# Kernel optimization log

Hardware: AMD Instinct MI355X
Metric: run time of the kernel (lower is better)

## Reference

```python
import jax, jax.numpy as jnp
import numpy as np

D = 2048
H = 16
DK = D // H
B = 2
S = 2048


def setup_inputs() -> dict:
    key = jax.random.key(0)
    ks = jax.random.split(key, 11)
    s = 1.0 / np.sqrt(D)
    inp = {
        "q": jax.random.normal(ks[0], (B, S, D), jnp.float32),
        "k": jax.random.normal(ks[1], (B, S, D), jnp.float32),
        "v": jax.random.normal(ks[2], (B, S, D), jnp.float32),
        "mask": 0,
        "Wq": jax.random.normal(ks[3], (D, D), jnp.float32) * s,
        "bq": jax.random.normal(ks[4], (D,), jnp.float32) * s,
        "Wk": jax.random.normal(ks[5], (D, D), jnp.float32) * s,
        "bk": jax.random.normal(ks[6], (D,), jnp.float32) * s,
        "Wv": jax.random.normal(ks[7], (D, D), jnp.float32) * s,
        "bv": jax.random.normal(ks[8], (D,), jnp.float32) * s,
        "Wo": jax.random.normal(ks[9], (D, D), jnp.float32) * s,
        "bo": jax.random.normal(ks[10], (D,), jnp.float32) * s,
    }
    return inp


def reference(q, k, v, mask, Wq, bq, Wk, bk, Wv, bv, Wo, bo):
    # Linear projections (torch Linear: x @ W.T + b)
    query = q @ Wq.T + bq  # [B,S,D]
    key_ = k @ Wk.T + bk
    value = v @ Wv.T + bv
    # split heads -> [B,S,H,DK]
    query = query.reshape(B, S, H, DK)
    key_ = key_.reshape(B, S, H, DK)
    value = value.reshape(B, S, H, DK)
    # scores [B,H,Sq,Sk]
    scores = jnp.einsum('nqhd,nkhd->nhqk', query, key_)
    if mask:
        # faithful to source: fill where triu(ones, diag=1) == 0 (lower tri incl diag)
        tri = jnp.triu(jnp.ones((S, S), jnp.float32), k=1)
        scores = jnp.where(tri == 0, jnp.float32(-1e20), scores)
    attn = jax.nn.softmax(scores / np.sqrt(DK), axis=3)
    # dropout=0.0 -> identity
    out = jnp.einsum('nhql,nlhd->nqhd', attn, value).reshape(B, S, D)
    return out @ Wo.T + bo
```

## Files before the change

### kernel.cpp

```cpp
#include <hip/hip_runtime.h>
#include <math.h>

typedef unsigned short u16;
typedef u16 u16x8 __attribute__((ext_vector_type(8)));
typedef u16 u16x4 __attribute__((ext_vector_type(4)));
typedef short s16x8 __attribute__((ext_vector_type(8)));
typedef short s16x4 __attribute__((ext_vector_type(4)));
typedef float f32x4 __attribute__((ext_vector_type(4)));

static constexpr int B_ = 2;
static constexpr int S_ = 2048;
static constexpr int D_ = 2048;
static constexpr int H_ = 16;
static constexpr int DK = 128;
static constexpr long long BSD = (long long)B_ * S_ * D_;
static constexpr long long DD  = (long long)D_ * D_;

#if __has_builtin(__builtin_amdgcn_mfma_f32_16x16x32_bf16)
#define HAVE_MFMA32 1
#else
#define HAVE_MFMA32 0
#endif
#if __has_builtin(__builtin_amdgcn_mfma_f32_16x16x16bf16_1k)
#define HAVE_MFMA16 1
#else
#define HAVE_MFMA16 0
#endif

__device__ __forceinline__ u16 f2bf(float f) {
    union { float f; unsigned u; } cv; cv.f = f;
    unsigned u = cv.u;
    return (u16)((u + 0x7fffu + ((u >> 16) & 1u)) >> 16);
}

__device__ __forceinline__ unsigned pack2bf(float a, float b) {
    union { float f; unsigned u; } x, y; x.f = a; y.f = b;
    return ((y.u + 0x8000u) & 0xffff0000u) | ((x.u + 0x8000u) >> 16);
}

__device__ __forceinline__ f32x4 mfma32(f32x4 c, u16x8 a, u16x8 b) {
#if HAVE_MFMA32
    return __builtin_amdgcn_mfma_f32_16x16x32_bf16((s16x8)a, (s16x8)b, c, 0, 0, 0);
#else
    asm volatile("v_mfma_f32_16x16x32_bf16 %0, %1, %2, %0" : "+v"(c) : "v"(a), "v"(b));
    return c;
#endif
}
__device__ __forceinline__ f32x4 mfma16(f32x4 c, u16x4 a, u16x4 b) {
#if HAVE_MFMA16
    return __builtin_amdgcn_mfma_f32_16x16x16bf16_1k((s16x4)a, (s16x4)b, c, 0, 0, 0);
#else
    asm volatile("v_mfma_f32_16x16x16_bf16 %0, %1, %2, %0" : "+v"(c) : "v"(a), "v"(b));
    return c;
#endif
}
__device__ __forceinline__ void fenceB() {
#if !HAVE_MFMA32 || !HAVE_MFMA16
    asm volatile("s_nop 7\ns_nop 7" :::);
#endif
}

__device__ __forceinline__ void glds16(const u16* g, u16* l) {
    __builtin_amdgcn_global_load_lds(
        (const __attribute__((address_space(1))) unsigned int*)g,
        (__attribute__((address_space(3))) unsigned int*)l, 16, 0, 0);
}

__device__ __forceinline__ float fexp2(float x) {
#if __has_builtin(__builtin_amdgcn_exp2f)
    return __builtin_amdgcn_exp2f(x);
#else
    return exp2f(x);
#endif
}

__device__ __forceinline__ void cfence() { asm volatile("" ::: "memory"); }
__device__ __forceinline__ void barrier8() {
    cfence();
    __builtin_amdgcn_s_barrier();
    cfence();
}
#define VMC(N)  asm volatile("s_waitcnt vmcnt(" #N ")" ::: "memory")
#define LGKMB() do { asm volatile("s_waitcnt lgkmcnt(0)" ::: "memory"); barrier8(); } while (0)

struct CastArgs {
    const float* src[7];
    u16* dst[7];
    int start[8];
};
__global__ __launch_bounds__(256) void cast_all(CastArgs a) {
    int g = blockIdx.x * 256 + threadIdx.x;
    if (g >= a.start[7]) return;
    int seg = 0;
#pragma unroll
    for (int i = 1; i < 7; ++i) seg += (g >= a.start[i]) ? 1 : 0;
    int idx = g - a.start[seg];
    float4 f = ((const float4*)a.src[seg])[idx];
    ushort4 o;
    o.x = f2bf(f.x); o.y = f2bf(f.y); o.z = f2bf(f.z); o.w = f2bf(f.w);
    ((ushort4*)a.dst[seg])[idx] = o;
}


#define ABYTE(s) ((s) * 16384)
#define BBYTE(s) (49152 + (s) * 32768)

#define STAGE_TILE(SA, SB)                                                          \
    glds16(pA0, SMu + ((SA) >> 1) + d0);                                            \
    glds16(pA1, SMu + ((SA) >> 1) + d1);                                            \
    glds16(pB00, SMu + ((SB) >> 1) + d0);                                           \
    glds16(pB01, SMu + ((SB) >> 1) + d1);                                           \
    glds16(pB10, SMu + ((SB) >> 1) + 8192 + d0);                                    \
    glds16(pB11, SMu + ((SB) >> 1) + 8192 + d1);                                    \
    pA0 += 64; pA1 += 64; pB00 += 64; pB01 += 64; pB10 += 64; pB11 += 64;

#define LD8(BOFF) (*(const u16x8*)(SMc + (BOFF)))

#define RD_FRAGS(SA, SB)                                                            \
    _Pragma("unroll")                                                               \
    for (int i2 = 0; i2 < 4; ++i2) {                                                \
        afA[i2] = LD8((SA) + offA[i2]);                                             \
        afB[i2] = LD8((SA) + (offA[i2] ^ 64));                                      \
    }                                                                               \
    _Pragma("unroll")                                                               \
    for (int j2 = 0; j2 < 4; ++j2) {                                                \
        bfA[j2] = LD8((SB) + offB[j2]);                                             \
        bfB[j2] = LD8((SB) + (offB[j2] ^ 64));                                      \
    }

#define MMALL()                                                                     \
    __builtin_amdgcn_s_setprio(1);                                                  \
    _Pragma("unroll")                                                               \
    for (int i2 = 0; i2 < 4; ++i2)                                                  \
        _Pragma("unroll")                                                           \
        for (int j2 = 0; j2 < 4; ++j2)                                              \
            acc[i2][j2] = mfma32(acc[i2][j2], afA[i2], bfA[j2]);                    \
    _Pragma("unroll")                                                               \
    for (int i2 = 0; i2 < 4; ++i2)                                                  \
        _Pragma("unroll")                                                           \
        for (int j2 = 0; j2 < 4; ++j2)                                              \
            acc[i2][j2] = mfma32(acc[i2][j2], afB[i2], bfB[j2]);                    \
    __builtin_amdgcn_s_setprio(0);

#define GEMM_LEAN_BODY(AGPTR, BGPTR)                                                \
    u16* const SMu = SM8;                                                           \
    const char* const SMc = (const char*)SM8;                                       \
    const int t = threadIdx.x;                                                      \
    const int lane = t & 63;                                                        \
    const int quad = lane >> 4, l16 = lane & 15;                                    \
    const int wave = t >> 6;                                                        \
    const int wm64 = (wave >> 2) * 64;                                              \
    const int wn64 = (wave & 3) * 64;                                               \
    const long long m0 = (long long)by * 128;                                       \
    const long long n0 = (long long)bx * 256;                                       \
    const int tr = t >> 3, tc = t & 7;                                              \
    const int swz = (tc ^ (tr & 7)) * 8;                                            \
    const u16* pA0  = (AGPTR) + (m0 + tr) * D_ + swz;                               \
    const u16* pA1  = (AGPTR) + (m0 + 64 + tr) * D_ + swz;                          \
    const u16* pB00 = (BGPTR) + (n0 + tr) * D_ + swz;                               \
    const u16* pB01 = (BGPTR) + (n0 + 64 + tr) * D_ + swz;                          \
    const u16* pB10 = (BGPTR) + (n0 + 128 + tr) * D_ + swz;                         \
    const u16* pB11 = (BGPTR) + (n0 + 192 + tr) * D_ + swz;                         \
    const int d0 = t * 8, d1 = t * 8 + 4096;                                        \
    int offA[4], offB[4];                                                           \
    _Pragma("unroll")                                                               \
    for (int i2 = 0; i2 < 4; ++i2) {                                                \
        int rowA = wm64 + i2 * 16 + l16;                                            \
        offA[i2] = rowA * 128 + ((quad ^ (rowA & 7)) << 4);                         \
        int rowB = wn64 + i2 * 16 + l16;                                            \
        offB[i2] = rowB * 128 + ((quad ^ (rowB & 7)) << 4);                         \
    }                                                                               \
    f32x4 acc[4][4];                                                                \
    _Pragma("unroll")                                                               \
    for (int i = 0; i < 4; ++i)                                                     \
        _Pragma("unroll")                                                           \
        for (int j = 0; j < 4; ++j)                                                 \
            acc[i][j] = f32x4{0.f, 0.f, 0.f, 0.f};                                  \
    u16x8 afA[4], afB[4], bfA[4], bfB[4];                                           \
                                            \
    STAGE_TILE(ABYTE(0), BBYTE(0))                                                  \
    STAGE_TILE(ABYTE(1), BBYTE(1))                                                  \
    VMC(6);                                                                         \
    barrier8();                                                                     \
    _Pragma("unroll 3")                                                             \
    for (int kt = 0; kt < 30; ++kt) {                                               \
        const int s = kt % 3;                                                       \
        const int s2 = (kt + 2) % 3;                                                \
        RD_FRAGS(ABYTE(s), BBYTE(s))                                                \
        STAGE_TILE(ABYTE(s2), BBYTE(s2))                                            \
        MMALL()                                                                     \
        VMC(6);                                                                     \
        LGKMB();                                                                    \
    }                                                                               \
                             \
    RD_FRAGS(ABYTE(0), BBYTE(0))                                                    \
    MMALL()                                                                         \
    VMC(0);                                                                         \
    LGKMB();                                                                        \
                                                              \
    RD_FRAGS(ABYTE(1), BBYTE(1))                                                    \
    MMALL()                                                                         \
    LGKMB();                                                                        \
    fenceB();

struct QkvArgs {
    const u16* X[3];
    const u16* W[3];
    const float* bias[3];
    u16* outQ;
    u16* outK;
    u16* outVt;
    float scaleQ;
};

__global__ __launch_bounds__(512, 2) void qkv_lean(QkvArgs a) {
    __shared__ u16 SM8[73728];

    const int l = blockIdx.x;
    const int zsel = l >> 8;
    const int pi = l & 7;
    const int cc_ = (l >> 3) & 31;
    const int by = (pi & 3) * 8 + (cc_ & 7);
    const int bx = ((pi >> 2) << 2) + (cc_ >> 3);

    const u16* __restrict__ Ag = a.X[zsel];
    const u16* __restrict__ Bg = a.W[zsel];

    GEMM_LEAN_BODY(Ag, Bg)

    float bs[4];
#pragma unroll
    for (int j = 0; j < 4; ++j)
        bs[j] = a.bias[zsel][(int)n0 + wn64 + j * 16 + l16];

    if (zsel < 2) {
        const float scale = (zsel == 0) ? a.scaleQ : 1.0f;
        u16* C = (zsel == 0) ? a.outQ : a.outK;
#pragma unroll
        for (int i = 0; i < 4; ++i)
#pragma unroll
            for (int j = 0; j < 4; ++j)
#pragma unroll
                for (int rr = 0; rr < 4; ++rr) {
                    int row = wm64 + i * 16 + quad * 4 + rr;
                    int col = wn64 + j * 16 + l16;
                    SM8[row * 256 + col] = f2bf((acc[i][j][rr] + bs[j]) * scale);
                }
        barrier8();
#pragma unroll
        for (int s = 0; s < 8; ++s) {
            int idx = s * 512 + t;
            int row = idx >> 5, c = idx & 31;
            *(u16x8*)(C + (m0 + row) * (long long)D_ + n0 + c * 8) =
                *(const u16x8*)(&SM8[row * 256 + c * 8]);
        }
    } else {
        const int h0 = (int)(n0 >> 7);
        const int bb = (int)(m0 >> 11);
        const int tok0 = (int)(m0 & 2047);
#pragma unroll
        for (int i = 0; i < 4; ++i)
#pragma unroll
            for (int j = 0; j < 4; ++j)
#pragma unroll
                for (int rr = 0; rr < 4; ++rr) {
                    int row = wm64 + i * 16 + quad * 4 + rr;
                    int d = wn64 + j * 16 + l16;
                    SM8[d * 136 + row] = f2bf(acc[i][j][rr] + bs[j]);
                }
        barrier8();
#pragma unroll
        for (int hh = 0; hh < 2; ++hh) {
            u16* vt = a.outVt + (long long)(bb * 16 + h0 + hh) * DK * S_;
#pragma unroll
            for (int s = 0; s < 4; ++s) {
                int idx = s * 512 + t;
                int d = idx >> 4, tcc = idx & 15;
                *(u16x8*)(vt + (long long)d * S_ + tok0 + tcc * 8) =
                    *(const u16x8*)(&SM8[(hh * 128 + d) * 136 + tcc * 8]);
            }
        }
    }
}

__global__ __launch_bounds__(512, 2) void gemm_out_lean(const u16* __restrict__ Ain,
                                                        const u16* __restrict__ Bin,
                                                        float* __restrict__ C,
                                                        const float* __restrict__ bias) {
    __shared__ u16 SM8[73728];

    const int l = blockIdx.x;
    const int pi = l & 7;
    const int cc_ = (l >> 3) & 31;
    const int by = (pi & 3) * 8 + (cc_ & 7);
    const int bx = ((pi >> 2) << 2) + (cc_ >> 3);

    GEMM_LEAN_BODY(Ain, Bin)

    float bs[4];
#pragma unroll
    for (int j = 0; j < 4; ++j)
        bs[j] = bias[(int)n0 + wn64 + j * 16 + l16];

    float* Cf = (float*)SM8;
#pragma unroll
    for (int p = 0; p < 2; ++p) {
        barrier8();
        if (((wave & 3) >> 1) == p) {
            int wnl = (wave & 1) * 64;
#pragma unroll
            for (int i = 0; i < 4; ++i)
#pragma unroll
                for (int j = 0; j < 4; ++j)
#pragma unroll
                    for (int rr = 0; rr < 4; ++rr) {
                        int row = wm64 + i * 16 + quad * 4 + rr;
                        int lc = wnl + j * 16 + l16;
                        Cf[row * 128 + lc] = acc[i][j][rr] + bs[j];
                    }
        }
        barrier8();
#pragma unroll
        for (int s = 0; s < 8; ++s) {
            int idx = s * 512 + t;
            int row = idx >> 5, c4 = idx & 31;
            f32x4 val = *(const f32x4*)(&Cf[row * 128 + c4 * 4]);
            *(f32x4*)(C + (m0 + row) * (long long)D_ + n0 + p * 128 + c4 * 4) = val;
        }
    }
}

__global__ __launch_bounds__(256, 2) void flash_attn(const u16* __restrict__ Qb,
                                                     const u16* __restrict__ Kb,
                                                     const u16* __restrict__ Vt,
                                                     u16* __restrict__ Ob) {
    __shared__ u16 Ks[2][64 * 128];
    __shared__ u16 Vs[2][128 * 64];

    const int z  = blockIdx.x;
    const int qt = blockIdx.y;
    const int b  = z >> 4, h = z & 15;
    const int t = threadIdx.x, wave = t >> 6, lane = t & 63;
    const int quad = lane >> 4, l16 = lane & 15;

    const u16* kbase = Kb + (long long)(b * S_) * D_ + h * DK;
    const u16* vbase = Vt + (long long)z * DK * S_;

    u16x8 qf[2][4];
    {
        const u16* qbase = Qb + ((long long)(b * S_ + qt * 128 + wave * 32 + l16)) * D_
                              + h * DK + quad * 8;
#pragma unroll
        for (int jq = 0; jq < 2; ++jq)
#pragma unroll
            for (int kk = 0; kk < 4; ++kk)
                qf[jq][kk] = *(const u16x8*)(qbase + (long long)jq * 16 * D_ + kk * 32);
    }

    f32x4 acc_o[2][8];
#pragma unroll
    for (int jq = 0; jq < 2; ++jq)
#pragma unroll
        for (int jd = 0; jd < 8; ++jd)
            acc_o[jq][jd] = f32x4{0.f, 0.f, 0.f, 0.f};
    float l_[2] = {0.f, 0.f};

    u16x8 vreg[4];

    {
#pragma unroll
        for (int i = 0; i < 4; ++i) {
            int slot = i * 256 + t;
            int row = slot >> 3, c16 = slot & 7;
            vreg[i] = *(const u16x8*)(vbase + (long long)row * S_ + c16 * 8);
        }
#pragma unroll
        for (int i = 0; i < 4; ++i) {
            int slot = i * 256 + t;
            int row = slot >> 4;
            int cs = (slot & 15) ^ (row & 7);
            glds16(kbase + (long long)row * D_ + cs * 8, &Ks[0][slot * 8]);
        }
#pragma unroll
        for (int i = 0; i < 4; ++i) {
            int slot = i * 256 + t;
            int row = slot >> 3, c16 = slot & 7;
            int rm = row & 15;
            u16x4 lo = __builtin_shufflevector(vreg[i], vreg[i], 0, 1, 2, 3);
            u16x4 hi = __builtin_shufflevector(vreg[i], vreg[i], 4, 5, 6, 7);
            *(u16x4*)(&Vs[0][row * 64 + (((2 * c16) ^ rm) * 4)]) = lo;
            *(u16x4*)(&Vs[0][row * 64 + (((2 * c16 + 1) ^ rm) * 4)]) = hi;
        }
    }

    for (int kt = 0; kt < S_ / 64; ++kt) {
        __syncthreads();
        const int p = kt & 1;
        const u16* ks = Ks[p];
        const u16* vs = Vs[p];
        const bool pre = (kt + 1) < (S_ / 64);
        if (pre) {
            const u16* vsrc = vbase + (kt + 1) * 64;
#pragma unroll
            for (int i = 0; i < 4; ++i) {
                int slot = i * 256 + t;
                int row = slot >> 3, c16 = slot & 7;
                vreg[i] = *(const u16x8*)(vsrc + (long long)row * S_ + c16 * 8);
            }
            const u16* ksrc = kbase + (long long)(kt + 1) * 64 * D_;
#pragma unroll
            for (int i = 0; i < 4; ++i) {
                int slot = i * 256 + t;
                int row = slot >> 4;
                int cs = (slot & 15) ^ (row & 7);
                glds16(ksrc + (long long)row * D_ + cs * 8, &Ks[p ^ 1][slot * 8]);
            }
        }

        f32x4 st[4][2];
#pragma unroll
        for (int ik = 0; ik < 4; ++ik)
#pragma unroll
            for (int jq = 0; jq < 2; ++jq)
                st[ik][jq] = f32x4{0.f, 0.f, 0.f, 0.f};
#pragma unroll
        for (int kk = 0; kk < 4; ++kk) {
            u16x8 kf[4];
#pragma unroll
            for (int ik = 0; ik < 4; ++ik) {
                int krow = ik * 16 + l16;
                kf[ik] = *(const u16x8*)(&ks[krow * 128 + (((kk * 4 + quad) ^ (l16 & 7)) * 8)]);
            }
#pragma unroll
            for (int ik = 0; ik < 4; ++ik) {
                st[ik][0] = mfma32(st[ik][0], kf[ik], qf[0][kk]);
                st[ik][1] = mfma32(st[ik][1], kf[ik], qf[1][kk]);
            }
        }
        fenceB();

        if (pre) {
#pragma unroll
            for (int i = 0; i < 4; ++i) {
                int slot = i * 256 + t;
                int row = slot >> 3, c16 = slot & 7;
                int rm = row & 15;
                u16x4 lo = __builtin_shufflevector(vreg[i], vreg[i], 0, 1, 2, 3);
                u16x4 hi = __builtin_shufflevector(vreg[i], vreg[i], 4, 5, 6, 7);
                *(u16x4*)(&Vs[p ^ 1][row * 64 + (((2 * c16) ^ rm) * 4)]) = lo;
                *(u16x4*)(&Vs[p ^ 1][row * 64 + (((2 * c16 + 1) ^ rm) * 4)]) = hi;
            }
        }

        u16x4 pf[4][2];
#pragma unroll
        for (int ik = 0; ik < 4; ++ik)
#pragma unroll
            for (int jq = 0; jq < 2; ++jq) {
                float p0 = fexp2(st[ik][jq][0]);
                float p1 = fexp2(st[ik][jq][1]);
                float p2 = fexp2(st[ik][jq][2]);
                float p3 = fexp2(st[ik][jq][3]);
                l_[jq] += (p0 + p1) + (p2 + p3);
                union { u16x4 v; unsigned u[2]; } pk;
                pk.u[0] = pack2bf(p0, p1);
                pk.u[1] = pack2bf(p2, p3);
                pf[ik][jq] = pk.v;
            }

#pragma unroll
        for (int ik = 0; ik < 4; ++ik) {
            const int kc = ik * 4 + quad;
            u16x4 vf[8];
#pragma unroll
            for (int jd = 0; jd < 8; ++jd) {
                int vrow = jd * 16 + l16;
                vf[jd] = *(const u16x4*)(&vs[vrow * 64 + ((kc ^ l16) * 4)]);
            }
#pragma unroll
            for (int jd = 0; jd < 8; ++jd) {
                acc_o[0][jd] = mfma16(acc_o[0][jd], pf[ik][0], vf[jd]);
                acc_o[1][jd] = mfma16(acc_o[1][jd], pf[ik][1], vf[jd]);
            }
        }
        fenceB();
    }

    float lr[2][4];
#pragma unroll
    for (int jq = 0; jq < 2; ++jq) {
        float s = l_[jq];
        s += __shfl_xor(s, 16, 64);
        s += __shfl_xor(s, 32, 64);
        float inv = 1.f / s;
#pragma unroll
        for (int r = 0; r < 4; ++r)
            lr[jq][r] = __shfl(inv, quad * 20 + r, 64);
    }
    u16* OS = (u16*)Ks;
    __syncthreads();
#pragma unroll
    for (int jq = 0; jq < 2; ++jq)
#pragma unroll
        for (int r = 0; r < 4; ++r) {
            int qloc = wave * 32 + jq * 16 + quad * 4 + r;
#pragma unroll
            for (int jd = 0; jd < 8; ++jd)
                OS[qloc * 128 + jd * 16 + l16] = f2bf(acc_o[jq][jd][r] * lr[jq][r]);
        }
    __syncthreads();
    u16* obase = Ob + ((long long)(b * S_ + qt * 128)) * D_ + h * DK;
#pragma unroll
    for (int i = 0; i < 8; ++i) {
        int idx = i * 256 + t;
        int row = idx >> 4, cc = idx & 15;
        *(u16x8*)(obase + (long long)row * D_ + cc * 8) = *(const u16x8*)(&OS[row * 128 + cc * 8]);
    }
}

extern "C" void kernel_launch(void* const* d_in, const int* in_sizes, int n_in,
                              void* d_out, int out_size, void* d_ws, size_t ws_size,
                              hipStream_t stream) {
    const float* q  = (const float*)d_in[0];
    const float* k  = (const float*)d_in[1];
    const float* v  = (const float*)d_in[2];
    const float* Wq = (const float*)d_in[4];
    const float* bq = (const float*)d_in[5];
    const float* Wk = (const float*)d_in[6];
    const float* bk = (const float*)d_in[7];
    const float* Wv = (const float*)d_in[8];
    const float* bv = (const float*)d_in[9];
    const float* Wo = (const float*)d_in[10];
    const float* bo = (const float*)d_in[11];
    float* out = (float*)d_out;

    u16* ws = (u16*)d_ws;
    u16* xq  = ws; ws += BSD;
    u16* xk  = ws; ws += BSD;
    u16* xv  = ws; ws += BSD;
    u16* wqb = ws; ws += DD;
    u16* wkb = ws; ws += DD;
    u16* wvb = ws; ws += DD;
    u16* wob = ws; ws += DD;
    u16* Qb  = ws; ws += BSD;
    u16* Kb  = ws; ws += BSD;
    u16* Vt  = ws; ws += BSD;
    u16* Ob  = ws; ws += BSD;

    const float q_scale = (float)(0.08838834764831845 * 1.4426950408889634);

    {
        CastArgs a;
        const float* srcs[7] = {q, k, v, Wq, Wk, Wv, Wo};
        u16* dsts[7] = {xq, xk, xv, wqb, wkb, wvb, wob};
        int n4s[7] = {(int)(BSD / 4), (int)(BSD / 4), (int)(BSD / 4),
                      (int)(DD / 4), (int)(DD / 4), (int)(DD / 4), (int)(DD / 4)};
        int acc = 0;
        for (int i = 0; i < 7; ++i) { a.src[i] = srcs[i]; a.dst[i] = dsts[i]; a.start[i] = acc; acc += n4s[i]; }
        a.start[7] = acc;
        cast_all<<<(acc + 255) / 256, 256, 0, stream>>>(a);
    }

    {
        QkvArgs a;
        a.X[0] = xq;  a.X[1] = xk;  a.X[2] = xv;
        a.W[0] = wqb; a.W[1] = wkb; a.W[2] = wvb;
        a.bias[0] = bq; a.bias[1] = bk; a.bias[2] = bv;
        a.outQ = Qb; a.outK = Kb; a.outVt = Vt;
        a.scaleQ = q_scale;
        qkv_lean<<<dim3(768, 1, 1), 512, 0, stream>>>(a);
    }

    flash_attn<<<dim3(B_ * H_, S_ / 128), 256, 0, stream>>>(Qb, Kb, Vt, Ob);

    gemm_out_lean<<<dim3(256, 1, 1), 512, 0, stream>>>(Ob, wob, out, bo);
}
```

Measured before the change: 428.2 us.

## Replace lean output GEMM with simple 128x128 single-buffered K64 tiled kernel

Swaps the output-projection GEMM from a 512-thread, 256-column-wide, multi-stage pipelined kernel with swizzled block ordering to a 256-thread 128x128 tile kernel. The new kernel loads A/B tiles with direct-to-LDS loads and an XOR swizzle, and syncs twice per K step without double buffering. It uses less shared memory per block, so more blocks can be resident and the grid is a plain 2D launch. It gives up the load/compute overlap and the L2-friendly block ordering of the previous kernel.

```diff
diff --git a/kernel.cpp b/kernel.cpp
--- a/kernel.cpp
+++ b/kernel.cpp
@@ -100,6 +100,50 @@
     o.x = f2bf(f.x); o.y = f2bf(f.y); o.z = f2bf(f.z); o.w = f2bf(f.w);
     ((ushort4*)a.dst[seg])[idx] = o;
 }
+
+#define GEMM_K64_LOOP(Aptr, Bptr)                                                   \
+    for (int k0 = 0; k0 < D_; k0 += 64) {                                           \
+        __syncthreads();                                                            \
+        _Pragma("unroll")                                                           \
+        for (int s = 0; s < 4; ++s) {                                               \
+            int slot = s * 256 + t;                                                 \
+            int row = slot >> 3;                                                    \
+            int c = (t & 7) ^ (row & 7);                                            \
+            glds16(Aptr + (m0 + row) * D_ + k0 + c * 8, &As[slot * 8]);             \
+        }                                                                           \
+        _Pragma("unroll")                                                           \
+        for (int s = 0; s < 4; ++s) {                                               \
+            int slot = s * 256 + t;                                                 \
+            int row = slot >> 3;                                                    \
+            int c = (t & 7) ^ (row & 7);                                            \
+            glds16(Bptr + (n0 + row) * D_ + k0 + c * 8, &Bs[slot * 8]);             \
+        }                                                                           \
+        __syncthreads();                                                            \
+        u16x8 af[4][2], bf[4][2];                                                   \
+        _Pragma("unroll")                                                           \
+        for (int i = 0; i < 4; ++i) {                                               \
+            int row = wm + i * 16 + l16;                                            \
+            _Pragma("unroll")                                                       \
+            for (int kk = 0; kk < 2; ++kk)                                          \
+                af[i][kk] = *(const u16x8*)(&As[row * 64 +                          \
+                                (((kk * 4 + quad) ^ (row & 7)) * 8)]);              \
+        }                                                                           \
+        _Pragma("unroll")                                                           \
+        for (int j = 0; j < 4; ++j) {                                               \
+            int row = wn + j * 16 + l16;                                            \
+            _Pragma("unroll")                                                       \
+            for (int kk = 0; kk < 2; ++kk)                                          \
+                bf[j][kk] = *(const u16x8*)(&Bs[row * 64 +                          \
+                                (((kk * 4 + quad) ^ (row & 7)) * 8)]);              \
+        }                                                                           \
+        _Pragma("unroll")                                                           \
+        for (int kk = 0; kk < 2; ++kk)                                              \
+            _Pragma("unroll")                                                       \
+            for (int i = 0; i < 4; ++i)                                             \
+                _Pragma("unroll")                                                   \
+                for (int j = 0; j < 4; ++j)                                         \
+                    acc[i][j] = mfma32(acc[i][j], af[i][kk], bf[j][kk]);            \
+    }
 
 
 #define ABYTE(s) ((s) * 16384)
@@ -283,49 +327,62 @@
     }
 }
 
-__global__ __launch_bounds__(512, 2) void gemm_out_lean(const u16* __restrict__ Ain,
-                                                        const u16* __restrict__ Bin,
-                                                        float* __restrict__ C,
-                                                        const float* __restrict__ bias) {
-    __shared__ u16 SM8[73728];
-
-    const int l = blockIdx.x;
-    const int pi = l & 7;
-    const int cc_ = (l >> 3) & 31;
-    const int by = (pi & 3) * 8 + (cc_ & 7);
-    const int bx = ((pi >> 2) << 2) + (cc_ >> 3);
-
-    GEMM_LEAN_BODY(Ain, Bin)
+__global__ __launch_bounds__(256) void gemm_out(const u16* __restrict__ Ain,
+                                                const u16* __restrict__ Bin,
+                                                float* __restrict__ C,
+                                                const float* __restrict__ bias) {
+    __shared__ u16 SM[16384];
+    u16* As = SM;
+    u16* Bs = SM + 8192;
+
+    const int t = threadIdx.x;
+    const int wave = t >> 6, lane = t & 63;
+    const int quad = lane >> 4, l16 = lane & 15;
+    const int wm = (wave >> 1) * 64;
+    const int wn = (wave & 1) * 64;
+    const long long m0 = (long long)blockIdx.y * 128;
+    const long long n0 = (long long)blockIdx.x * 128;
+
+    f32x4 acc[4][4];
+#pragma unroll
+    for (int i = 0; i < 4; ++i)
+#pragma unroll
+        for (int j = 0; j < 4; ++j)
+            acc[i][j] = f32x4{0.f, 0.f, 0.f, 0.f};
+
+    GEMM_K64_LOOP(Ain, Bin)
+
+    fenceB();
 
     float bs[4];
 #pragma unroll
     for (int j = 0; j < 4; ++j)
-        bs[j] = bias[(int)n0 + wn64 + j * 16 + l16];
-
-    float* Cf = (float*)SM8;
+        bs[j] = bias[(int)n0 + wn + j * 16 + l16];
+
+    float* Cf = (float*)SM;
 #pragma unroll
     for (int p = 0; p < 2; ++p) {
-        barrier8();
-        if (((wave & 3) >> 1) == p) {
-            int wnl = (wave & 1) * 64;
+        __syncthreads();
+#pragma unroll
+        for (int jj = 0; jj < 2; ++jj) {
+            int j = p * 2 + jj;
 #pragma unroll
             for (int i = 0; i < 4; ++i)
 #pragma unroll
-                for (int j = 0; j < 4; ++j)
-#pragma unroll
-                    for (int rr = 0; rr < 4; ++rr) {
-                        int row = wm64 + i * 16 + quad * 4 + rr;
-                        int lc = wnl + j * 16 + l16;
-                        Cf[row * 128 + lc] = acc[i][j][rr] + bs[j];
-                    }
-        }
-        barrier8();
-#pragma unroll
-        for (int s = 0; s < 8; ++s) {
-            int idx = s * 512 + t;
-            int row = idx >> 5, c4 = idx & 31;
-            f32x4 val = *(const f32x4*)(&Cf[row * 128 + c4 * 4]);
-            *(f32x4*)(C + (m0 + row) * (long long)D_ + n0 + p * 128 + c4 * 4) = val;
+                for (int r = 0; r < 4; ++r) {
+                    int row = wm + i * 16 + quad * 4 + r;
+                    int lc = (wave & 1) * 32 + jj * 16 + l16;
+                    Cf[row * 64 + lc] = acc[i][j][r] + bs[j];
+                }
+        }
+        __syncthreads();
+#pragma unroll
+        for (int i = 0; i < 8; ++i) {
+            int idx = i * 256 + t;
+            int row = idx >> 4, c4 = idx & 15;
+            f32x4 val = *(const f32x4*)(&Cf[row * 64 + c4 * 4]);
+            long long n = n0 + (c4 >> 3) * 64 + p * 32 + (c4 & 7) * 4;
+            *(f32x4*)(C + (m0 + row) * (long long)D_ + n) = val;
         }
     }
 }
@@ -573,5 +630,5 @@
 
     flash_attn<<<dim3(B_ * H_, S_ / 128), 256, 0, stream>>>(Qb, Kb, Vt, Ob);
 
-    gemm_out_lean<<<dim3(256, 1, 1), 512, 0, stream>>>(Ob, wob, out, bo);
-}
+    gemm_out<<<dim3(D_ / 128, (B_ * S_) / 128), 256, 0, stream>>>(Ob, wob, out, bo);
+}
```

Measured after the change: 411.8 us. -3.8%, faster.
